# Kernel optimization log

Measured on AMD Instinct MI355X. Metric: run time of the kernel, lower is better.

The kernel has to match this reference:

```python
import jax, jax.numpy as jnp
import numpy as np

B, T, C, H = 4, 2048, 1024, 16
HS = C // H  # head_size = 64


def setup_inputs() -> dict:
    key = jax.random.key(0)
    ks = jax.random.split(key, 6)
    s = C ** -0.5  # Linear default init scale (approx, kaiming-uniform-ish)
    x = jax.random.normal(ks[0], (B, T, C), dtype=jnp.float32)
    Wq = jax.random.normal(ks[1], (H, C, HS), dtype=jnp.float32) * s
    Wk = jax.random.normal(ks[2], (H, C, HS), dtype=jnp.float32) * s
    Wv = jax.random.normal(ks[3], (H, C, HS), dtype=jnp.float32) * s
    Wproj = jax.random.normal(ks[4], (C, C), dtype=jnp.float32) * s
    bproj = jax.random.normal(ks[5], (C,), dtype=jnp.float32) * s
    return {"x": x, "Wq": Wq, "Wk": Wk, "Wv": Wv, "Wproj": Wproj, "bproj": bproj}


def reference(x, Wq, Wk, Wv, Wproj, bproj):
    # Batched multi-head attention equivalent to looping over per-head modules.
    # q,k,v: (B, H, T, HS)
    q = jnp.einsum('btc,hcd->bhtd', x, Wq)
    k = jnp.einsum('btc,hcd->bhtd', x, Wk)
    v = jnp.einsum('btc,hcd->bhtd', x, Wv)
    scale = HS ** -0.5
    scores = jnp.einsum('bhqd,bhkd->bhqk', q, k) * scale  # (B,H,T,T)
    causal = jnp.tril(jnp.ones((T, T), dtype=bool))
    scores = jnp.where(causal, scores, -jnp.inf)
    wei = jax.nn.softmax(scores, axis=-1)
    out_heads = jnp.einsum('bhqk,bhkd->bhqd', wei, v)  # (B,H,T,HS)
    # concat heads along last dim -> (B,T,H*HS) = (B,T,C)
    combo = out_heads.transpose(0, 2, 1, 3).reshape(B, T, C)
    out = jnp.einsum('btc,cd->btd', combo, Wproj.T.T @ jnp.eye(C, dtype=combo.dtype)) if False else combo @ Wproj.T + bproj
    # dropout p=0.0 (eval) -> identity
    return out
```

## Files before the change

kernel.cpp:

```cpp
#include <hip/hip_runtime.h>
#include <stdint.h>

#define B_  4
#define T_  2048
#define C_  1024
#define H_  16
#define HS_ 64
#define M_  (B_*T_)
#define K_  C_

typedef unsigned short u16;
typedef float v4f __attribute__((ext_vector_type(4)));
typedef short v8s __attribute__((ext_vector_type(8)));
typedef u16   v4u __attribute__((ext_vector_type(4)));
typedef unsigned int u32;
typedef u32 v2u32 __attribute__((ext_vector_type(2)));

__device__ __forceinline__ u16 f2bf(float f){
  unsigned u = __float_as_uint(f);
  u += 0x7fffu + ((u >> 16) & 1u);
  return (u16)(u >> 16);
}

__device__ __forceinline__ u32 cvt_pk_bf16(float a, float b){
  u32 r;
  asm("v_cvt_pk_bf16_f32 %0, %1, %2" : "=v"(r) : "v"(a), "v"(b));
  return r;
}

__device__ __forceinline__ void async16(const void* g, void* l){
  __builtin_amdgcn_global_load_lds(
      (const __attribute__((address_space(1))) unsigned int*)g,
      (__attribute__((address_space(3))) unsigned int*)l,
      16, 0, 0);
}

__global__ void conv_f32_bf16(const float* __restrict__ src, u16* __restrict__ dst){
  int i = (blockIdx.x * 256 + threadIdx.x) * 4;
  v4f v = *(const v4f*)(src + i);
  v4u o;
  #pragma unroll
  for (int j = 0; j < 4; j++) o[j] = f2bf(v[j]);
  *(v4u*)(dst + i) = o;
}

__global__ void transpose_w(const float* __restrict__ Wq, const float* __restrict__ Wk,
                            const float* __restrict__ Wv, u16* __restrict__ wallT){
  int idx = blockIdx.x * 256 + threadIdx.x;
  int n = idx >> 10, c = idx & 1023;
  int tensor = n >> 10;
  int h = (n >> 6) & 15;
  int d = n & 63;
  const float* W = (tensor == 0) ? Wq : ((tensor == 1) ? Wk : Wv);
  wallT[idx] = f2bf(W[((size_t)(h * C_ + c)) * HS_ + d]);
}

#define QSCALE 0.1803368801111204f

template<int MODE>
__global__ __launch_bounds__(256)
void gemm_bt(const u16* __restrict__ A, const u16* __restrict__ Bt,
             const float* __restrict__ bias,
             u16* __restrict__ o0, u16* __restrict__ o1, u16* __restrict__ o2,
             float* __restrict__ o0f)
{
  __shared__ __align__(16) u16 sA[128 * 32];
  __shared__ __align__(16) u16 sB[128 * 32];
  const int tid  = threadIdx.x;
  const int lane = tid & 63;
  const int wave = tid >> 6;
  const int l15  = lane & 15, quad = lane >> 4;
  const int wm   = wave >> 1, wn = wave & 1;
  const int m0   = blockIdx.y * 128;
  const int n0   = blockIdx.x * 128;

  v4f acc[4][4] = {};

  const int L0 = tid * 16;
  const int r0 = L0 >> 6, c0 = L0 & 63;
  const int L1 = (256 + tid) * 16;
  const int r1 = L1 >> 6, c1 = L1 & 63;

  const char* Ab = (const char*)A;
  const char* Bb = (const char*)Bt;

  for (int kk = 0; kk < K_; kk += 32){
    async16(Ab + ((size_t)(m0 + r0) * K_ + kk) * 2 + c0, (char*)sA + L0);
    async16(Ab + ((size_t)(m0 + r1) * K_ + kk) * 2 + c1, (char*)sA + L1);
    async16(Bb + ((size_t)(n0 + r0) * K_ + kk) * 2 + c0, (char*)sB + L0);
    async16(Bb + ((size_t)(n0 + r1) * K_ + kk) * 2 + c1, (char*)sB + L1);
    __syncthreads();

    v8s af[4], bfr[4];
    #pragma unroll
    for (int mi = 0; mi < 4; mi++)
      af[mi] = *(const v8s*)(sA + (wm * 64 + mi * 16 + l15) * 32 + quad * 8);
    #pragma unroll
    for (int ni = 0; ni < 4; ni++)
      bfr[ni] = *(const v8s*)(sB + (wn * 64 + ni * 16 + l15) * 32 + quad * 8);

    #pragma unroll
    for (int mi = 0; mi < 4; mi++)
      #pragma unroll
      for (int ni = 0; ni < 4; ni++)
        acc[mi][ni] = __builtin_amdgcn_mfma_f32_16x16x32_bf16(af[mi], bfr[ni], acc[mi][ni], 0, 0, 0);
    __syncthreads();
  }

  if constexpr (MODE == 0){
    #pragma unroll
    for (int ni = 0; ni < 4; ni++){
      const int ng = n0 + wn * 64 + ni * 16 + l15;
      const int tensor = ng >> 10;
      const int hh = (ng >> 6) & 15;
      const int d  = ng & 63;
      #pragma unroll
      for (int mi = 0; mi < 4; mi++){
        const int mbase = m0 + wm * 64 + mi * 16 + quad * 4;
        const int bb = mbase >> 11;
        const int tt = mbase & 2047;
        if (tensor == 2){
          v4u pk;
          #pragma unroll
          for (int r = 0; r < 4; r++) pk[r] = f2bf(acc[mi][ni][r]);
          *(v4u*)(o2 + ((size_t)((bb * H_ + hh) * HS_ + d)) * T_ + tt) = pk;
        } else if (tensor == 0){
          #pragma unroll
          for (int r = 0; r < 4; r++)
            o0[((size_t)((bb * H_ + hh)) * T_ + tt + r) * HS_ + d] = f2bf(acc[mi][ni][r] * QSCALE);
        } else {
          #pragma unroll
          for (int r = 0; r < 4; r++)
            o1[((size_t)((bb * H_ + hh)) * T_ + tt + r) * HS_ + d] = f2bf(acc[mi][ni][r]);
        }
      }
    }
  } else {
    #pragma unroll
    for (int ni = 0; ni < 4; ni++){
      const int ng = n0 + wn * 64 + ni * 16 + l15;
      const float bv = bias[ng];
      #pragma unroll
      for (int mi = 0; mi < 4; mi++){
        const int mbase = m0 + wm * 64 + mi * 16 + quad * 4;
        #pragma unroll
        for (int r = 0; r < 4; r++)
          o0f[(size_t)(mbase + r) * C_ + ng] = acc[mi][ni][r] + bv;
      }
    }
  }
}

__global__ __launch_bounds__(512, 4)
void attn(const u16* __restrict__ Q, const u16* __restrict__ Kb_, const u16* __restrict__ Vt,
          u16* __restrict__ O)
{
  __shared__ __align__(16) u16 sK[64 * 64];
  __shared__ __align__(16) u16 sV[64 * 64];
  __shared__ __align__(16) u16 Plds[8][16][80];
  const int tid  = threadIdx.x;
  const int lane = tid & 63;
  const int wave = tid >> 6;
  const int l15  = lane & 15, quad = lane >> 4;
  const int pp   = blockIdx.y & 7;
  const int bh   = blockIdx.x * 8 + (blockIdx.y >> 3);

  const u16* Qb = Q   + (size_t)bh * T_ * HS_;
  const u16* Kb = Kb_ + (size_t)bh * T_ * HS_;
  const u16* Vb = Vt  + (size_t)bh * HS_ * T_;
  const int b = bh >> 4, h = bh & 15;

  const int g  = tid;
  const int tg = g >> 3;
  const int sw = ((g & 7) ^ (tg & 7)) << 4;
  const char* Kby = (const char*)Kb;
  const char* Vby = (const char*)Vb;
  const int koff = tg * 128 + sw;
  const int voff = tg * (T_ * 2) + sw;
  char* sKp = (char*)sK + g * 16;
  char* sVp = (char*)sV + g * 16;

  const int fsw0 = (quad ^ (l15 & 7)) * 8;
  const int fsw1 = ((quad + 4) ^ (l15 & 7)) * 8;

  #pragma unroll 1
  for (int ph = 0; ph < 2; ph++){
    const int qt = ph ? (15 - pp) : pp;
    const int q0 = qt * 128 + wave * 16;

    const v8s qf0 = *(const v8s*)(Qb + (size_t)(q0 + l15) * HS_ + quad * 8);
    const v8s qf1 = *(const v8s*)(Qb + (size_t)(q0 + l15) * HS_ + 32 + quad * 8);

    v4f Oa[4] = {};
    float lsum = 0.f;

    const int ktmax = 2 * qt + 1;
    for (int kt = 0; kt <= ktmax; kt++){
      const int k0 = kt * 64;
      async16(Kby + (size_t)k0 * 128 + koff, sKp);
      async16(Vby + (size_t)k0 * 2   + voff, sVp);
      __syncthreads();

      if (k0 <= q0 + 15){
        v4f sacc[4] = {};
        #pragma unroll
        for (int nt = 0; nt < 4; nt++){
          const u16* kr = sK + (nt * 16 + l15) * 64;
          v8s kf0 = *(const v8s*)(kr + fsw0);
          v8s kf1 = *(const v8s*)(kr + fsw1);
          sacc[nt] = __builtin_amdgcn_mfma_f32_16x16x32_bf16(kf0, qf0, sacc[nt], 0, 0, 0);
          sacc[nt] = __builtin_amdgcn_mfma_f32_16x16x32_bf16(kf1, qf1, sacc[nt], 0, 0, 0);
        }
        const bool diag = (k0 + 63 > q0);
        const int qrow_rel = (q0 - k0) + l15;

        #pragma unroll
        for (int nt = 0; nt < 4; nt++){
          float p0 = exp2f(sacc[nt][0]);
          float p1 = exp2f(sacc[nt][1]);
          float p2 = exp2f(sacc[nt][2]);
          float p3 = exp2f(sacc[nt][3]);
          if (diag){
            const int kbase = nt * 16 + quad * 4;
            if (kbase + 0 > qrow_rel) p0 = 0.f;
            if (kbase + 1 > qrow_rel) p1 = 0.f;
            if (kbase + 2 > qrow_rel) p2 = 0.f;
            if (kbase + 3 > qrow_rel) p3 = 0.f;
          }
          lsum += (p0 + p1) + (p2 + p3);
          v2u32 w;
          w[0] = cvt_pk_bf16(p0, p1);
          w[1] = cvt_pk_bf16(p2, p3);
          *(v2u32*)&Plds[wave][l15][nt * 16 + quad * 4] = w;
        }

        asm volatile("" ::: "memory");
        const v8s pf0 = *(const v8s*)&Plds[wave][l15][quad * 8];
        const v8s pf1 = *(const v8s*)&Plds[wave][l15][32 + quad * 8];
        #pragma unroll
        for (int nt = 0; nt < 4; nt++){
          const u16* vr = sV + (nt * 16 + l15) * 64;
          v8s vf0 = *(const v8s*)(vr + fsw0);
          v8s vf1 = *(const v8s*)(vr + fsw1);
          Oa[nt] = __builtin_amdgcn_mfma_f32_16x16x32_bf16(pf0, vf0, Oa[nt], 0, 0, 0);
          Oa[nt] = __builtin_amdgcn_mfma_f32_16x16x32_bf16(pf1, vf1, Oa[nt], 0, 0, 0);
        }
      }
      __syncthreads();
    }

    float rs = lsum;
    rs += __shfl_xor(rs, 16);
    rs += __shfl_xor(rs, 32);
    #pragma unroll
    for (int reg = 0; reg < 4; reg++){
      const float rsq = __shfl(rs, quad * 4 + reg);
      const float inv = (rsq > 0.f) ? (1.f / rsq) : 0.f;
      const int t = q0 + quad * 4 + reg;
      #pragma unroll
      for (int nt = 0; nt < 4; nt++)
        O[((size_t)(b * T_ + t)) * C_ + h * HS_ + nt * 16 + l15] = f2bf(Oa[nt][reg] * inv);
    }
  }
}

extern "C" void kernel_launch(void* const* d_in, const int* in_sizes, int n_in,
                              void* d_out, int out_size, void* d_ws, size_t ws_size,
                              hipStream_t stream)
{
  const float* x     = (const float*)d_in[0];
  const float* Wq    = (const float*)d_in[1];
  const float* Wk    = (const float*)d_in[2];
  const float* Wv    = (const float*)d_in[3];
  const float* Wproj = (const float*)d_in[4];
  const float* bproj = (const float*)d_in[5];
  float* out = (float*)d_out;

  u16* xhat   = (u16*)d_ws;
  u16* att    = xhat;
  u16* q_ws   = xhat  + (size_t)M_ * C_;
  u16* k_ws   = q_ws  + (size_t)M_ * C_;
  u16* vt_ws  = k_ws  + (size_t)M_ * C_;
  u16* wallT  = vt_ws + (size_t)M_ * C_;
  u16* wprojT = wallT + (size_t)3 * C_ * K_;

  conv_f32_bf16<<<dim3((M_ * C_) / 1024), dim3(256), 0, stream>>>(x, xhat);
  transpose_w<<<dim3((3 * C_ * K_) / 256), dim3(256), 0, stream>>>(Wq, Wk, Wv, wallT);
  conv_f32_bf16<<<dim3((C_ * C_) / 1024), dim3(256), 0, stream>>>(Wproj, wprojT);
  gemm_bt<0><<<dim3(24, 64), dim3(256), 0, stream>>>(xhat, wallT, nullptr,
                                                     q_ws, k_ws, vt_ws, nullptr);
  attn<<<dim3(8, 64), dim3(512), 0, stream>>>(q_ws, k_ws, vt_ws, att);
  gemm_bt<1><<<dim3(8, 64), dim3(256), 0, stream>>>(att, wprojT, bproj,
                                                    nullptr, nullptr, nullptr, out);
}
```

Measured before the change: 281.6 us.

## Process two 16-row query tiles per wave in attention with half the threads

The attention kernel now runs 4 waves per block instead of 8, and each wave handles two 16-row query sub-tiles. Each K/V fragment read from LDS is reused for both sub-tiles, and each thread issues two async loads per K/V tile. MFMA sections are wrapped in s_setprio to favour matrix issue. The aim is to cut LDS read traffic per FLOP and barrier overhead per unit of work, at the cost of more registers and fewer waves to hide latency.

```diff
diff --git a/kernel.cpp b/kernel.cpp
--- a/kernel.cpp
+++ b/kernel.cpp
@@ -151,13 +151,13 @@
   }
 }
 
-__global__ __launch_bounds__(512, 4)
+__global__ __launch_bounds__(256, 4)
 void attn(const u16* __restrict__ Q, const u16* __restrict__ Kb_, const u16* __restrict__ Vt,
           u16* __restrict__ O)
 {
   __shared__ __align__(16) u16 sK[64 * 64];
   __shared__ __align__(16) u16 sV[64 * 64];
-  __shared__ __align__(16) u16 Plds[8][16][80];
+  __shared__ __align__(16) u16 Plds[4][32][80];
   const int tid  = threadIdx.x;
   const int lane = tid & 63;
   const int wave = tid >> 6;
@@ -170,15 +170,16 @@
   const u16* Vb = Vt  + (size_t)bh * HS_ * T_;
   const int b = bh >> 4, h = bh & 15;
 
-  const int g  = tid;
-  const int tg = g >> 3;
-  const int sw = ((g & 7) ^ (tg & 7)) << 4;
+  const int g0 = tid, g1 = tid + 256;
+  const int t0g = g0 >> 3, t1g = g1 >> 3;
+  const int sw0 = ((g0 & 7) ^ (t0g & 7)) << 4;
+  const int sw1 = ((g1 & 7) ^ (t1g & 7)) << 4;
   const char* Kby = (const char*)Kb;
   const char* Vby = (const char*)Vb;
-  const int koff = tg * 128 + sw;
-  const int voff = tg * (T_ * 2) + sw;
-  char* sKp = (char*)sK + g * 16;
-  char* sVp = (char*)sV + g * 16;
+  const int koff0 = t0g * 128 + sw0,        koff1 = t1g * 128 + sw1;
+  const int voff0 = t0g * (T_ * 2) + sw0,   voff1 = t1g * (T_ * 2) + sw1;
+  char* sKp0 = (char*)sK + g0 * 16;  char* sKp1 = (char*)sK + g1 * 16;
+  char* sVp0 = (char*)sV + g0 * 16;  char* sVp1 = (char*)sV + g1 * 16;
 
   const int fsw0 = (quad ^ (l15 & 7)) * 8;
   const int fsw1 = ((quad + 4) ^ (l15 & 7)) * 8;
@@ -186,80 +187,145 @@
   #pragma unroll 1
   for (int ph = 0; ph < 2; ph++){
     const int qt = ph ? (15 - pp) : pp;
-    const int q0 = qt * 128 + wave * 16;
-
-    const v8s qf0 = *(const v8s*)(Qb + (size_t)(q0 + l15) * HS_ + quad * 8);
-    const v8s qf1 = *(const v8s*)(Qb + (size_t)(q0 + l15) * HS_ + 32 + quad * 8);
-
-    v4f Oa[4] = {};
-    float lsum = 0.f;
+    const int q0a = qt * 128 + wave * 32;
+    const int q0b = q0a + 16;
+
+    const v8s qf0a = *(const v8s*)(Qb + (size_t)(q0a + l15) * HS_ + quad * 8);
+    const v8s qf1a = *(const v8s*)(Qb + (size_t)(q0a + l15) * HS_ + 32 + quad * 8);
+    const v8s qf0b = *(const v8s*)(Qb + (size_t)(q0b + l15) * HS_ + quad * 8);
+    const v8s qf1b = *(const v8s*)(Qb + (size_t)(q0b + l15) * HS_ + 32 + quad * 8);
+
+    v4f Oaa[4] = {}, Oab[4] = {};
+    float lsumA = 0.f, lsumB = 0.f;
 
     const int ktmax = 2 * qt + 1;
     for (int kt = 0; kt <= ktmax; kt++){
       const int k0 = kt * 64;
-      async16(Kby + (size_t)k0 * 128 + koff, sKp);
-      async16(Vby + (size_t)k0 * 2   + voff, sVp);
+      async16(Kby + (size_t)k0 * 128 + koff0, sKp0);
+      async16(Kby + (size_t)k0 * 128 + koff1, sKp1);
+      async16(Vby + (size_t)k0 * 2   + voff0, sVp0);
+      async16(Vby + (size_t)k0 * 2   + voff1, sVp1);
       __syncthreads();
 
-      if (k0 <= q0 + 15){
-        v4f sacc[4] = {};
+      if (k0 <= q0b + 15){
+        const bool actA = (k0 <= q0a + 15);
+
+        v4f sa[4] = {}, sb[4] = {};
+        __builtin_amdgcn_s_setprio(1);
         #pragma unroll
         for (int nt = 0; nt < 4; nt++){
           const u16* kr = sK + (nt * 16 + l15) * 64;
           v8s kf0 = *(const v8s*)(kr + fsw0);
           v8s kf1 = *(const v8s*)(kr + fsw1);
-          sacc[nt] = __builtin_amdgcn_mfma_f32_16x16x32_bf16(kf0, qf0, sacc[nt], 0, 0, 0);
-          sacc[nt] = __builtin_amdgcn_mfma_f32_16x16x32_bf16(kf1, qf1, sacc[nt], 0, 0, 0);
-        }
-        const bool diag = (k0 + 63 > q0);
-        const int qrow_rel = (q0 - k0) + l15;
-
-        #pragma unroll
-        for (int nt = 0; nt < 4; nt++){
-          float p0 = exp2f(sacc[nt][0]);
-          float p1 = exp2f(sacc[nt][1]);
-          float p2 = exp2f(sacc[nt][2]);
-          float p3 = exp2f(sacc[nt][3]);
-          if (diag){
-            const int kbase = nt * 16 + quad * 4;
-            if (kbase + 0 > qrow_rel) p0 = 0.f;
-            if (kbase + 1 > qrow_rel) p1 = 0.f;
-            if (kbase + 2 > qrow_rel) p2 = 0.f;
-            if (kbase + 3 > qrow_rel) p3 = 0.f;
+          sb[nt] = __builtin_amdgcn_mfma_f32_16x16x32_bf16(kf0, qf0b, sb[nt], 0, 0, 0);
+          sb[nt] = __builtin_amdgcn_mfma_f32_16x16x32_bf16(kf1, qf1b, sb[nt], 0, 0, 0);
+          if (actA){
+            sa[nt] = __builtin_amdgcn_mfma_f32_16x16x32_bf16(kf0, qf0a, sa[nt], 0, 0, 0);
+            sa[nt] = __builtin_amdgcn_mfma_f32_16x16x32_bf16(kf1, qf1a, sa[nt], 0, 0, 0);
           }
-          lsum += (p0 + p1) + (p2 + p3);
-          v2u32 w;
-          w[0] = cvt_pk_bf16(p0, p1);
-          w[1] = cvt_pk_bf16(p2, p3);
-          *(v2u32*)&Plds[wave][l15][nt * 16 + quad * 4] = w;
+        }
+        __builtin_amdgcn_s_setprio(0);
+
+        {
+          const bool diagB = (k0 + 63 > q0b);
+          const int qrelB = (q0b - k0) + l15;
+          #pragma unroll
+          for (int nt = 0; nt < 4; nt++){
+            float p0 = exp2f(sb[nt][0]);
+            float p1 = exp2f(sb[nt][1]);
+            float p2 = exp2f(sb[nt][2]);
+            float p3 = exp2f(sb[nt][3]);
+            if (diagB){
+              const int kbase = nt * 16 + quad * 4;
+              if (kbase + 0 > qrelB) p0 = 0.f;
+              if (kbase + 1 > qrelB) p1 = 0.f;
+              if (kbase + 2 > qrelB) p2 = 0.f;
+              if (kbase + 3 > qrelB) p3 = 0.f;
+            }
+            lsumB += (p0 + p1) + (p2 + p3);
+            v2u32 w;
+            w[0] = cvt_pk_bf16(p0, p1);
+            w[1] = cvt_pk_bf16(p2, p3);
+            *(v2u32*)&Plds[wave][16 + l15][nt * 16 + quad * 4] = w;
+          }
+        }
+        if (actA){
+          const bool diagA = (k0 + 63 > q0a);
+          const int qrelA = (q0a - k0) + l15;
+          #pragma unroll
+          for (int nt = 0; nt < 4; nt++){
+            float p0 = exp2f(sa[nt][0]);
+            float p1 = exp2f(sa[nt][1]);
+            float p2 = exp2f(sa[nt][2]);
+            float p3 = exp2f(sa[nt][3]);
+            if (diagA){
+              const int kbase = nt * 16 + quad * 4;
+              if (kbase + 0 > qrelA) p0 = 0.f;
+              if (kbase + 1 > qrelA) p1 = 0.f;
+              if (kbase + 2 > qrelA) p2 = 0.f;
+              if (kbase + 3 > qrelA) p3 = 0.f;
+            }
+            lsumA += (p0 + p1) + (p2 + p3);
+            v2u32 w;
+            w[0] = cvt_pk_bf16(p0, p1);
+            w[1] = cvt_pk_bf16(p2, p3);
+            *(v2u32*)&Plds[wave][l15][nt * 16 + quad * 4] = w;
+          }
         }
 
         asm volatile("" ::: "memory");
-        const v8s pf0 = *(const v8s*)&Plds[wave][l15][quad * 8];
-        const v8s pf1 = *(const v8s*)&Plds[wave][l15][32 + quad * 8];
+        const v8s pf0b = *(const v8s*)&Plds[wave][16 + l15][quad * 8];
+        const v8s pf1b = *(const v8s*)&Plds[wave][16 + l15][32 + quad * 8];
+        v8s pf0a, pf1a;
+        if (actA){
+          pf0a = *(const v8s*)&Plds[wave][l15][quad * 8];
+          pf1a = *(const v8s*)&Plds[wave][l15][32 + quad * 8];
+        }
+        __builtin_amdgcn_s_setprio(1);
         #pragma unroll
         for (int nt = 0; nt < 4; nt++){
           const u16* vr = sV + (nt * 16 + l15) * 64;
           v8s vf0 = *(const v8s*)(vr + fsw0);
           v8s vf1 = *(const v8s*)(vr + fsw1);
-          Oa[nt] = __builtin_amdgcn_mfma_f32_16x16x32_bf16(pf0, vf0, Oa[nt], 0, 0, 0);
-          Oa[nt] = __builtin_amdgcn_mfma_f32_16x16x32_bf16(pf1, vf1, Oa[nt], 0, 0, 0);
-        }
+          Oab[nt] = __builtin_amdgcn_mfma_f32_16x16x32_bf16(pf0b, vf0, Oab[nt], 0, 0, 0);
+          Oab[nt] = __builtin_amdgcn_mfma_f32_16x16x32_bf16(pf1b, vf1, Oab[nt], 0, 0, 0);
+          if (actA){
+            Oaa[nt] = __builtin_amdgcn_mfma_f32_16x16x32_bf16(pf0a, vf0, Oaa[nt], 0, 0, 0);
+            Oaa[nt] = __builtin_amdgcn_mfma_f32_16x16x32_bf16(pf1a, vf1, Oaa[nt], 0, 0, 0);
+          }
+        }
+        __builtin_amdgcn_s_setprio(0);
       }
       __syncthreads();
     }
 
-    float rs = lsum;
-    rs += __shfl_xor(rs, 16);
-    rs += __shfl_xor(rs, 32);
-    #pragma unroll
-    for (int reg = 0; reg < 4; reg++){
-      const float rsq = __shfl(rs, quad * 4 + reg);
-      const float inv = (rsq > 0.f) ? (1.f / rsq) : 0.f;
-      const int t = q0 + quad * 4 + reg;
-      #pragma unroll
-      for (int nt = 0; nt < 4; nt++)
-        O[((size_t)(b * T_ + t)) * C_ + h * HS_ + nt * 16 + l15] = f2bf(Oa[nt][reg] * inv);
+    {
+      float rs = lsumB;
+      rs += __shfl_xor(rs, 16);
+      rs += __shfl_xor(rs, 32);
+      #pragma unroll
+      for (int reg = 0; reg < 4; reg++){
+        const float rsq = __shfl(rs, quad * 4 + reg);
+        const float inv = (rsq > 0.f) ? (1.f / rsq) : 0.f;
+        const int t = q0b + quad * 4 + reg;
+        #pragma unroll
+        for (int nt = 0; nt < 4; nt++)
+          O[((size_t)(b * T_ + t)) * C_ + h * HS_ + nt * 16 + l15] = f2bf(Oab[nt][reg] * inv);
+      }
+    }
+    {
+      float rs = lsumA;
+      rs += __shfl_xor(rs, 16);
+      rs += __shfl_xor(rs, 32);
+      #pragma unroll
+      for (int reg = 0; reg < 4; reg++){
+        const float rsq = __shfl(rs, quad * 4 + reg);
+        const float inv = (rsq > 0.f) ? (1.f / rsq) : 0.f;
+        const int t = q0a + quad * 4 + reg;
+        #pragma unroll
+        for (int nt = 0; nt < 4; nt++)
+          O[((size_t)(b * T_ + t)) * C_ + h * HS_ + nt * 16 + l15] = f2bf(Oaa[nt][reg] * inv);
+      }
     }
   }
 }
@@ -289,7 +355,7 @@
   conv_f32_bf16<<<dim3((C_ * C_) / 1024), dim3(256), 0, stream>>>(Wproj, wprojT);
   gemm_bt<0><<<dim3(24, 64), dim3(256), 0, stream>>>(xhat, wallT, nullptr,
                                                      q_ws, k_ws, vt_ws, nullptr);
-  attn<<<dim3(8, 64), dim3(512), 0, stream>>>(q_ws, k_ws, vt_ws, att);
+  attn<<<dim3(8, 64), dim3(256), 0, stream>>>(q_ws, k_ws, vt_ws, att);
   gemm_bt<1><<<dim3(8, 64), dim3(256), 0, stream>>>(att, wprojT, bproj,
                                                     nullptr, nullptr, nullptr, out);
 }
```

Result: slower. 300.5 us (+6.7%).
